# Performance work log

Measured on AMD Instinct MI355X. Metric: run time of the kernel, lower is better.

## Reference

```python
import jax, jax.numpy as jnp
import numpy as np

WIN = 12     # SAMv3 window_size
HEADS = 8    # num_heads

def _window(t, win=WIN):
    B, H, W, C = t.shape
    t = t.reshape(B, H // win, win, W // win, win, C).transpose(0, 1, 3, 2, 4, 5)
    return t.reshape(B, (H // win) * (W // win), win * win, C)

def _unwindow(t, H, W, win=WIN):
    B, nW, S, C = t.shape
    t = t.reshape(B, H // win, W // win, win, win, C).transpose(0, 1, 3, 2, 4, 5)
    return t.reshape(B, H, W, C)

def _sam(fq, fkv, bias, wq, wk, wv, wo, bo):
    # Windowed, masked cross-frame multi-head attention (SAMv3).
    # fq, fkv: (B, C, H, W); bias: (B, nW, 1, 1, S) additive mask bias.
    B, C, H, W = fq.shape
    hd = C // HEADS
    scale = hd ** -0.5
    q = _window(jnp.einsum('bchw,cd->bhwd', fq, wq))   # (B,nW,S,C)
    k = _window(jnp.einsum('bchw,cd->bhwd', fkv, wk))
    v = _window(jnp.einsum('bchw,cd->bhwd', fkv, wv))
    nW, S = q.shape[1], q.shape[2]
    q = q.reshape(B, nW, S, HEADS, hd)
    k = k.reshape(B, nW, S, HEADS, hd)
    v = v.reshape(B, nW, S, HEADS, hd)
    attn = jnp.einsum('bnqhd,bnkhd->bnhqk', q, k) * scale + bias
    attn = jax.nn.softmax(attn, axis=-1)
    out = jnp.einsum('bnhqk,bnkhd->bnqhd', attn, v).reshape(B, nW, S, C)
    out = out @ wo + bo
    return _unwindow(out, H, W).transpose(0, 3, 1, 2)  # (B, C, H, W)

def setup_inputs() -> dict:
    key = jax.random.key(0)
    B, C, T, H, W = 2, 384, 2, 192, 192
    ks = jax.random.split(key, 16)
    d = {}
    d['x'] = jax.random.normal(ks[0], (B, C, T, H, W), jnp.float32)
    d['mask'] = jax.random.randint(ks[1], (B, T, 1, H, W), 0, 2, jnp.int32)
    names = ['sam1_wq', 'sam1_wk', 'sam1_wv', 'sam1_wo',
             'sam2_wq', 'sam2_wk', 'sam2_wv', 'sam2_wo',
             'proj1_w', 'proj2_w']
    for i, n in enumerate(names):
        d[n] = jax.random.normal(ks[2 + i], (C, C), jnp.float32) * 0.02
    d['sam1_bo'] = jnp.zeros((C,), jnp.float32)
    d['sam2_bo'] = jnp.zeros((C,), jnp.float32)
    d['proj1_b'] = jnp.zeros((C,), jnp.float32)
    d['proj2_b'] = jnp.zeros((C,), jnp.float32)
    return d

def reference(x, mask, sam1_wq, sam1_wk, sam1_wv, sam1_wo, sam1_bo,
              sam2_wq, sam2_wk, sam2_wv, sam2_wo, sam2_bo,
              proj1_w, proj1_b, proj2_w, proj2_b):
    # x: (B, C, T=2, H, W); mask: (B, T, 1, H, W)
    f1 = x[:, :, 0]
    f2 = x[:, :, 1]
    m = mask[:, 1, 0][..., None]                      # (B, H, W, 1), frame-2 mask
    mw = _window(m)[..., 0]                           # (B, nW, S)
    bias = jnp.where(mw == 0, -1e9, 0.0).astype(x.dtype)[:, :, None, None, :]
    o1 = _sam(f1, f2, bias, sam1_wq, sam1_wk, sam1_wv, sam1_wo, sam1_bo)
    x1 = jnp.einsum('bchw,dc->bdhw', o1, proj1_w) + proj1_b[None, :, None, None]
    o2 = _sam(f2, f1, bias, sam2_wq, sam2_wk, sam2_wv, sam2_wo, sam2_bo)
    x2 = jnp.einsum('bchw,dc->bdhw', o2, proj2_w) + proj2_b[None, :, None, None]
    return jnp.concatenate([x1[:, :, None], x2[:, :, None]], axis=2)  # (B, C, 2, H, W)
```

## Files before the change

### kernel.cpp

```cpp
#include <hip/hip_runtime.h>
#include <stdint.h>

typedef __attribute__((ext_vector_type(8))) short bf16x8;
typedef __attribute__((ext_vector_type(4))) float f32x4;

#define HW    36864
#define CCH   384
#define NPIX  73728
#define W2    147456
#define NPAD  1280
#define WTF   491520

__device__ __forceinline__ unsigned short f2bf(float f) {
  unsigned u = __builtin_bit_cast(unsigned, f);
  u += 0x7FFFu + ((u >> 16) & 1u);
  return (unsigned short)(u >> 16);
}

typedef const unsigned int __attribute__((address_space(1)))* gas1_t;
typedef unsigned int __attribute__((address_space(3)))* las3_t;
__device__ __forceinline__ void gload16(const void* g, void* l) {
  __builtin_amdgcn_global_load_lds((gas1_t)g, (las3_t)l, 16, 0, 0);
}


__global__ void k_wt(const float* __restrict__ w0, const float* __restrict__ w1,
                     const float* __restrict__ w2, const float* __restrict__ w3,
                     const float* __restrict__ w4, const float* __restrict__ w5,
                     unsigned short* __restrict__ wt) {
  int idx = blockIdx.x * 256 + threadIdx.x;
  int w = blockIdx.y;
  const float* W;
  switch (w) { case 0: W = w0; break; case 1: W = w1; break;
               case 2: W = w2; break; case 3: W = w3; break;
               case 4: W = w4; break; default: W = w5; break; }
  const int fmap[6]    = {0, 1, 1, 1, 0, 0};
  const int basemap[6] = {0, 384, 768, 0, 384, 768};
  int c = idx / 384, d = idx % 384;
  wt[(size_t)fmap[w] * WTF + (size_t)(basemap[w] + d) * 384 + c] =
      f2bf(W[(size_t)c * 384 + d]);
}

__global__ void k_pad(unsigned short* __restrict__ wt) {
  int idx = blockIdx.x * 256 + threadIdx.x;
  int f = idx / 49152, rem = idx % 49152;
  wt[(size_t)f * WTF + 1152 * 384 + rem] = 0;
}

__global__ void k_wf(const float* __restrict__ wo1, const float* __restrict__ pj1,
                     const float* __restrict__ wo2, const float* __restrict__ pj2,
                     unsigned short* __restrict__ wfT) {
  int idx = blockIdx.x * 256 + threadIdx.x;
  int s = blockIdx.y;
  const float* wo = s ? wo2 : wo1;
  const float* pj = s ? pj2 : pj1;
  int d = idx / 384, e = idx % 384;
  float acc = 0.f;
  for (int c = 0; c < 384; ++c) acc += pj[d * 384 + c] * wo[e * 384 + c];
  wfT[(size_t)s * W2 + (size_t)d * 384 + e] = f2bf(acc);
}

__global__ void k_bf(const float* __restrict__ bo1, const float* __restrict__ pj1,
                     const float* __restrict__ pb1, const float* __restrict__ bo2,
                     const float* __restrict__ pj2, const float* __restrict__ pb2,
                     float* __restrict__ bfused) {
  int t = threadIdx.x;
  int s = t / 384, d = t % 384;
  const float* bo = s ? bo2 : bo1;
  const float* pj = s ? pj2 : pj1;
  const float* pb = s ? pb2 : pb1;
  float acc = pb[d];
  for (int c = 0; c < 384; ++c) acc += pj[d * 384 + c] * bo[c];
  bfused[t] = acc;
}

__global__ __launch_bounds__(256) void k_tx(const float* __restrict__ x,
                                            unsigned short* __restrict__ xbf) {
  __shared__ float tile[64][65];
  int p0 = blockIdx.x * 64;
  int c0 = blockIdx.y * 64;
  int bt = blockIdx.z;
  int b = bt >> 1, t = bt & 1;
  int tid = threadIdx.x;
  int cl = tid >> 2;
  int pq = (tid & 3) * 4;
  const float* src = x + (((size_t)b * CCH + (c0 + cl)) * 2 + t) * HW + p0;
#pragma unroll
  for (int i = 0; i < 4; ++i) {
    int p_l = pq + i * 16;
    float4 v = *reinterpret_cast<const float4*>(src + p_l);
    tile[cl][p_l + 0] = v.x; tile[cl][p_l + 1] = v.y;
    tile[cl][p_l + 2] = v.z; tile[cl][p_l + 3] = v.w;
  }
  __syncthreads();
  int pl = tid >> 2;
  int cq = (tid & 3) * 16;
  unsigned short* dst = xbf + ((size_t)(t * 2 + b) * HW + p0 + pl) * CCH + c0 + cq;
  bf16x8 o0, o1;
#pragma unroll
  for (int j = 0; j < 8; ++j) o0[j] = (short)f2bf(tile[cq + j][pl]);
#pragma unroll
  for (int j = 0; j < 8; ++j) o1[j] = (short)f2bf(tile[cq + 8 + j][pl]);
  *reinterpret_cast<bf16x8*>(dst) = o0;
  *reinterpret_cast<bf16x8*>(dst + 8) = o1;
}

__global__ __launch_bounds__(512) void gemm_qkv(
    const unsigned short* __restrict__ xbf,
    const unsigned short* __restrict__ wt,
    unsigned short* __restrict__ qb0,
    unsigned short* __restrict__ qb1,
    unsigned short* __restrict__ kvb0,
    unsigned short* __restrict__ kvb1,
    float oscale) {
  __shared__ __align__(16) unsigned short Lsh[2][32768];
  const int tid = threadIdx.x;
  const int lane = tid & 63;
  const int wid = tid >> 6;
  const int wr = wid >> 2, wc = wid & 3;
  const int r15 = lane & 15, g = lane >> 4;
  const int rsw = r15 & 7;

  const int gx = gridDim.x;
  const int nwg = gx * gridDim.y;
  const int bid = blockIdx.x + blockIdx.y * gx;
  const int chunk = nwg >> 3;
  const int l = (bid & 7) * chunk + (bid >> 3);
  const int bx = l % gx, by = l / gx;

  const int f = (by >= 288) ? 1 : 0;
  const int m0 = (by - f * 288) * 256;
  const int n0 = bx * 256;

  const unsigned short* A  = xbf + (size_t)f * NPIX * 384;
  const unsigned short* Bt = wt + (size_t)f * WTF;
  unsigned short* Cq  = f ? qb1 : qb0;
  unsigned short* Ckv = f ? kvb0 : kvb1;

  const int gsl = (tid & 7) ^ ((tid >> 3) & 7);
  const unsigned short* srcA = A + (size_t)(m0 + (tid >> 3)) * 384 + gsl * 8;
  const unsigned short* srcB = Bt + (size_t)(n0 + (tid >> 3)) * 384 + gsl * 8;

  f32x4 acc[8][4];
  f32x4 zero4 = {0.f, 0.f, 0.f, 0.f};
#pragma unroll
  for (int a = 0; a < 8; ++a)
#pragma unroll
    for (int b = 0; b < 4; ++b) acc[a][b] = zero4;

#define SA(buf, kt, q) gload16(srcA + (size_t)(q) * 64 * 384 + (kt) * 64, \
                               &Lsh[(buf)][tid * 8 + (q) * 4096])
#define SB(buf, kt, q) gload16(srcB + (size_t)(q) * 64 * 384 + (kt) * 64, \
                               &Lsh[(buf)][16384 + tid * 8 + (q) * 4096])

  bf16x8 af[4][2], bf[2][2];
#define LDA(buf, mh) do {                                                        \
    _Pragma("unroll")                                                            \
    for (int a = 0; a < 4; ++a) {                                                \
      int row = wr * 128 + (mh) * 64 + a * 16 + r15;                             \
      af[a][0] = *(const bf16x8*)&Lsh[(buf)][row * 64 + ((0 + g) ^ rsw) * 8];    \
      af[a][1] = *(const bf16x8*)&Lsh[(buf)][row * 64 + ((4 + g) ^ rsw) * 8];    \
    } } while (0)
#define LDB(buf, nh) do {                                                        \
    _Pragma("unroll")                                                            \
    for (int b = 0; b < 2; ++b) {                                                \
      int row = wc * 64 + (nh) * 32 + b * 16 + r15;                              \
      bf[b][0] = *(const bf16x8*)&Lsh[(buf)][16384 + row * 64 + ((0 + g) ^ rsw) * 8];\
      bf[b][1] = *(const bf16x8*)&Lsh[(buf)][16384 + row * 64 + ((4 + g) ^ rsw) * 8];\
    } } while (0)
#define MM(mh, nh) do {                                                          \
    __builtin_amdgcn_s_setprio(1);                                               \
    _Pragma("unroll")                                                            \
    for (int a = 0; a < 4; ++a)                                                  \
      _Pragma("unroll")                                                          \
      for (int b = 0; b < 2; ++b) {                                              \
        acc[(mh)*4+a][(nh)*2+b] = __builtin_amdgcn_mfma_f32_16x16x32_bf16(       \
            af[a][0], bf[b][0], acc[(mh)*4+a][(nh)*2+b], 0, 0, 0);               \
        acc[(mh)*4+a][(nh)*2+b] = __builtin_amdgcn_mfma_f32_16x16x32_bf16(       \
            af[a][1], bf[b][1], acc[(mh)*4+a][(nh)*2+b], 0, 0, 0);               \
      }                                                                          \
    __builtin_amdgcn_s_setprio(0);                                               \
  } while (0)

#define BAR() __builtin_amdgcn_s_barrier()
#define LGKM0() asm volatile("s_waitcnt lgkmcnt(0)" ::: "memory")

  SB(0, 0, 0); SB(0, 0, 1); SB(0, 0, 2); SB(0, 0, 3);
  SA(0, 0, 0); SA(0, 0, 2);
  SA(0, 0, 1); SA(0, 0, 3);
  asm volatile("s_waitcnt vmcnt(2)" ::: "memory");
  BAR();

#define TILE(kt, STG, W1STR, W3)                                              \
  do {                                                                        \
    const int c_ = (kt) & 1, s_ = c_ ^ 1;                                     \
    LDA(c_, 0); LDB(c_, 0);                                                   \
    if (STG) { SB(s_, (kt) + 1, 0); SB(s_, (kt) + 1, 1); }                    \
    BAR(); LGKM0(); MM(0, 0); BAR();                                          \
    LDB(c_, 1);                                                               \
    if (STG) { SB(s_, (kt) + 1, 2); SB(s_, (kt) + 1, 3); }                    \
    BAR(); LGKM0(); MM(0, 1);                                                 \
    asm volatile("s_waitcnt " W1STR ::: "memory");                            \
    BAR();                                                                    \
    LDA(c_, 1);                                                               \
    if (STG) { SA(s_, (kt) + 1, 0); SA(s_, (kt) + 1, 2); }                    \
    BAR(); LGKM0(); MM(1, 1); BAR();                                          \
    LDB(c_, 0);                                                               \
    if (STG) { SA(s_, (kt) + 1, 1); SA(s_, (kt) + 1, 3); }                    \
    BAR(); LGKM0(); MM(1, 0);                                                 \
    if (W3) { asm volatile("s_waitcnt vmcnt(2)" ::: "memory"); BAR(); }       \
  } while (0)

  TILE(0, 1, "vmcnt(4)", 1);
  TILE(1, 1, "vmcnt(4)", 1);
  TILE(2, 1, "vmcnt(4)", 1);
  TILE(3, 1, "vmcnt(4)", 1);
  TILE(4, 1, "vmcnt(4)", 1);
  TILE(5, 0, "vmcnt(0)", 0);
#undef TILE
#undef SA
#undef SB
#undef LDA
#undef LDB
#undef MM
#undef BAR
#undef LGKM0

#pragma unroll
  for (int a = 0; a < 8; ++a) {
    int m = m0 + wr * 128 + a * 16 + g * 4;
#pragma unroll
    for (int b = 0; b < 4; ++b) {
      int nbase = n0 + wc * 64 + b * 16;
      if (nbase < 384) {
        unsigned short* cp = Cq + (size_t)m * 384 + nbase + r15;
#pragma unroll
        for (int r = 0; r < 4; ++r) cp[(size_t)r * 384] = f2bf(acc[a][b][r] * oscale);
      } else if (nbase < 1152) {
        unsigned short* cp = Ckv + (size_t)m * 768 + (nbase - 384) + r15;
#pragma unroll
        for (int r = 0; r < 4; ++r) cp[(size_t)r * 768] = f2bf(acc[a][b][r]);
      }
    }
  }
}

__global__ __launch_bounds__(256) void gemm_out(
    const unsigned short* __restrict__ wfT,
    const unsigned short* __restrict__ ob0,
    const unsigned short* __restrict__ ob1,
    float* __restrict__ Cf,
    const float* __restrict__ bfu) {
  __shared__ __align__(16) unsigned short Lsh[3][8192];
  const int tid = threadIdx.x;
  const int lane = tid & 63;
  const int wid = tid >> 6, wr = wid >> 1, wc = wid & 1;

  const int gx = gridDim.x, gy = gridDim.y;
  const int nwg = gx * gy * gridDim.z;
  const int bid = blockIdx.x + (blockIdx.y + blockIdx.z * gy) * gx;
  const int chunk = nwg >> 3;
  const int l = (bid & 7) * chunk + (bid >> 3);
  const int bx = l % gx;
  const int by = (l / gx) % gy;
  const int s  = l / (gx * gy);

  const unsigned short* A  = wfT + (size_t)s * W2;
  const unsigned short* Bt = s ? ob1 : ob0;
  const float* bias = bfu + s * 384;

  const int m0 = bx * 128;
  const int n0 = by * 128;
  const int r15 = lane & 15, g = lane >> 4;

  const int u1 = tid + 256;
  const unsigned short* srcA0 = A + (size_t)(m0 + (tid >> 2)) * 384 + (((tid & 3) ^ ((tid >> 3) & 3)) << 3);
  const unsigned short* srcA1 = A + (size_t)(m0 + (u1 >> 2)) * 384 + (((u1 & 3) ^ ((u1 >> 3) & 3)) << 3);
  const unsigned short* srcB0 = Bt + (size_t)(n0 + (tid >> 2)) * 384 + (((tid & 3) ^ ((tid >> 3) & 3)) << 3);
  const unsigned short* srcB1 = Bt + (size_t)(n0 + (u1 >> 2)) * 384 + (((u1 & 3) ^ ((u1 >> 3) & 3)) << 3);
  const int wbase = (tid & ~63) * 8;

  f32x4 acc[4][4];
  f32x4 zero4 = {0.f, 0.f, 0.f, 0.f};
#pragma unroll
  for (int a = 0; a < 4; ++a)
#pragma unroll
    for (int b = 0; b < 4; ++b) acc[a][b] = zero4;

  const int swzr = (g ^ ((r15 >> 1) & 3)) << 3;

#define STAGE(buf, kt) do {                                  \
    int ke = (kt) * 32;                                      \
    gload16(srcA0 + ke, &Lsh[(buf)][wbase]);                 \
    gload16(srcA1 + ke, &Lsh[(buf)][2048 + wbase]);          \
    gload16(srcB0 + ke, &Lsh[(buf)][4096 + wbase]);          \
    gload16(srcB1 + ke, &Lsh[(buf)][6144 + wbase]);          \
  } while (0)

#define COMPUTE(buf) do {                                                       \
    bf16x8 af[4], bfv[4];                                                       \
    _Pragma("unroll")                                                           \
    for (int a = 0; a < 4; ++a)                                                 \
      af[a] = *(const bf16x8*)&Lsh[(buf)][(wr * 64 + a * 16 + r15) * 32 + swzr];\
    _Pragma("unroll")                                                           \
    for (int b = 0; b < 4; ++b)                                                 \
      bfv[b] = *(const bf16x8*)&Lsh[(buf)][4096 + (wc * 64 + b * 16 + r15) * 32 + swzr];\
    _Pragma("unroll")                                                           \
    for (int a = 0; a < 4; ++a)                                                 \
      _Pragma("unroll")                                                         \
      for (int b = 0; b < 4; ++b)                                               \
        acc[a][b] = __builtin_amdgcn_mfma_f32_16x16x32_bf16(af[a], bfv[b], acc[a][b], 0, 0, 0);\
  } while (0)

  STAGE(0, 0);
  STAGE(1, 1);
#pragma unroll
  for (int kt = 0; kt < 11; ++kt) {
    asm volatile("s_waitcnt vmcnt(4)" ::: "memory");
    __builtin_amdgcn_s_barrier();
    asm volatile("" ::: "memory");
    if (kt < 10) STAGE((kt + 2) % 3, kt + 2);
    COMPUTE(kt % 3);
  }
  __syncthreads();
  COMPUTE(11 % 3);
#undef STAGE
#undef COMPUTE

  int bb = n0 / HW;
#pragma unroll
  for (int a = 0; a < 4; ++a) {
    int d = m0 + wr * 64 + a * 16 + g * 4;
#pragma unroll
    for (int b = 0; b < 4; ++b) {
      int n = n0 + wc * 64 + b * 16 + r15;
      int p = n - bb * HW;
#pragma unroll
      for (int r = 0; r < 4; ++r) {
        float v = acc[a][b][r] + bias[d + r];
        Cf[(((size_t)bb * CCH + (d + r)) * 2 + s) * HW + p] = v;
      }
    }
  }
}

__global__ __launch_bounds__(512, 2) void attn_kernel(
    const unsigned short* __restrict__ qb0,
    const unsigned short* __restrict__ qb1,
    const unsigned short* __restrict__ kvb0,
    const unsigned short* __restrict__ kvb1,
    const int* __restrict__ mask,
    unsigned short* __restrict__ ob0,
    unsigned short* __restrict__ ob1) {
  __shared__ __align__(16) unsigned short P[8][16][168];
  __shared__ int ptab[144];
  const int n = blockIdx.x, b = blockIdx.y, s = blockIdx.z;
  const unsigned short* q  = s ? qb1 : qb0;
  const unsigned short* kv = s ? kvb1 : kvb0;
  unsigned short* obuf = s ? ob1 : ob0;
  const int tid = threadIdx.x;
  const int h = tid >> 6, lane = tid & 63;
  const int c15 = lane & 15, g = lane >> 4;
  const int wy = n >> 4, wx = n & 15;
  const size_t rowbase = (size_t)b * HW;
  const int* mrow = mask + (size_t)(b * 2 + 1) * HW;

  if (tid < 144)
    ptab[tid] = (wy * 12 + tid / 12) * 192 + wx * 12 + tid % 12;

  for (int idx = lane; idx < 16 * 24; idx += 64)
    P[h][idx / 24][144 + (idx % 24)] = 0;
  __syncthreads();

  float biasv[9];
#pragma unroll
  for (int nt = 0; nt < 9; ++nt)
    biasv[nt] = (mrow[ptab[nt * 16 + c15]] == 0) ? -1e9f : 0.0f;

  bf16x8 zfrag = {0, 0, 0, 0, 0, 0, 0, 0};
  f32x4 zero4 = {0.f, 0.f, 0.f, 0.f};

  bf16x8 kf0[9], kf1[9];
#pragma unroll
  for (int nt = 0; nt < 9; ++nt) {
    const unsigned short* kp = kv + (rowbase + ptab[nt * 16 + c15]) * 768 + h * 48;
    kf0[nt] = *(const bf16x8*)(kp + g * 8);
    kf1[nt] = zfrag;
    if (g < 2) kf1[nt] = *(const bf16x8*)(kp + 32 + g * 8);
  }

  const unsigned short* vb = kv + rowbase * 768 + 384 + h * 48;
  bf16x8 vf[5][3];
#pragma unroll
  for (int ks = 0; ks < 5; ++ks) {
#pragma unroll
    for (int dt = 0; dt < 3; ++dt) {
      bf16x8 v = {0, 0, 0, 0, 0, 0, 0, 0};
#pragma unroll
      for (int j = 0; j < 8; ++j) {
        int sk = ks * 32 + g * 8 + j;
        if (sk < 144)
          v[j] = (short)vb[(size_t)ptab[sk] * 768 + dt * 16 + c15];
      }
      vf[ks][dt] = v;
    }
  }

  bf16x8 qf0, qf1;
  {
    const unsigned short* qp = q + (rowbase + ptab[c15]) * 384 + h * 48;
    qf0 = *(const bf16x8*)(qp + g * 8);
    qf1 = zfrag;
    if (g < 2) qf1 = *(const bf16x8*)(qp + 32 + g * 8);
  }

  for (int mt = 0; mt < 9; ++mt) {
    bf16x8 qn0 = zfrag, qn1 = zfrag;
    if (mt < 8) {
      const unsigned short* qp = q + (rowbase + ptab[(mt + 1) * 16 + c15]) * 384 + h * 48;
      qn0 = *(const bf16x8*)(qp + g * 8);
      if (g < 2) qn1 = *(const bf16x8*)(qp + 32 + g * 8);
    }

    float l4[4] = {0.f, 0.f, 0.f, 0.f};
    f32x4 oacc[3];
#pragma unroll
    for (int dt = 0; dt < 3; ++dt) oacc[dt] = zero4;

#pragma unroll
    for (int nt = 0; nt < 9; ++nt) {
      f32x4 sv = __builtin_amdgcn_mfma_f32_16x16x32_bf16(qf1, kf1[nt], zero4, 0, 0, 0);
      sv = __builtin_amdgcn_mfma_f32_16x16x32_bf16(qf0, kf0[nt], sv, 0, 0, 0);
#pragma unroll
      for (int r = 0; r < 4; ++r) {
        float pv = __expf(sv[r] + biasv[nt]);
        l4[r] += pv;
        P[h][g * 4 + r][nt * 16 + c15] = f2bf(pv);
      }
      if (nt & 1) {
        int ks = nt >> 1;
        bf16x8 pf = *(const bf16x8*)&P[h][c15][ks * 32 + g * 8];
#pragma unroll
        for (int dt = 0; dt < 3; ++dt)
          oacc[dt] = __builtin_amdgcn_mfma_f32_16x16x32_bf16(pf, vf[ks][dt], oacc[dt], 0, 0, 0);
      }
    }
    {
      bf16x8 pf = *(const bf16x8*)&P[h][c15][4 * 32 + g * 8];
#pragma unroll
      for (int dt = 0; dt < 3; ++dt)
        oacc[dt] = __builtin_amdgcn_mfma_f32_16x16x32_bf16(pf, vf[4][dt], oacc[dt], 0, 0, 0);
    }

#pragma unroll
    for (int st = 1; st < 16; st <<= 1)
#pragma unroll
      for (int r = 0; r < 4; ++r) l4[r] += __shfl_xor(l4[r], st, 64);

    float inv[4];
#pragma unroll
    for (int r = 0; r < 4; ++r) inv[r] = 1.0f / l4[r];
#pragma unroll
    for (int dt = 0; dt < 3; ++dt) {
#pragma unroll
      for (int r = 0; r < 4; ++r) {
        int so = mt * 16 + g * 4 + r;
        obuf[(rowbase + ptab[so]) * 384 + h * 48 + dt * 16 + c15] =
            f2bf(oacc[dt][r] * inv[r]);
      }
    }

    qf0 = qn0; qf1 = qn1;
  }
}

extern "C" void kernel_launch(void* const* d_in, const int* in_sizes, int n_in,
                              void* d_out, int out_size, void* d_ws, size_t ws_size,
                              hipStream_t stream) {
  const float* x    = (const float*)d_in[0];
  const int*   mask = (const int*)d_in[1];
  const float* wq1 = (const float*)d_in[2];
  const float* wk1 = (const float*)d_in[3];
  const float* wv1 = (const float*)d_in[4];
  const float* wo1 = (const float*)d_in[5];
  const float* wq2 = (const float*)d_in[6];
  const float* wk2 = (const float*)d_in[7];
  const float* wv2 = (const float*)d_in[8];
  const float* wo2 = (const float*)d_in[9];
  const float* pj1 = (const float*)d_in[10];
  const float* pj2 = (const float*)d_in[11];
  const float* bo1 = (const float*)d_in[12];
  const float* bo2 = (const float*)d_in[13];
  const float* pb1 = (const float*)d_in[14];
  const float* pb2 = (const float*)d_in[15];
  float* out = (float*)d_out;

  const float SCALE = 0.14433756729740643f;

  char* ws = (char*)d_ws;
  size_t off = 0;
  unsigned short* wt   = (unsigned short*)(ws + off); off += (size_t)2 * WTF * 2;
  unsigned short* wfT  = (unsigned short*)(ws + off); off += (size_t)2 * W2 * 2;
  float*          bfu  = (float*)(ws + off);          off += (size_t)2 * 384 * 4;
  unsigned short* xbf  = (unsigned short*)(ws + off); off += (size_t)4 * HW * CCH * 2;
  size_t qsz = (size_t)NPIX * 384 * 2, kvsz = (size_t)NPIX * 768 * 2;
  unsigned short* qb0  = (unsigned short*)(ws + off); off += qsz;
  unsigned short* qb1  = (unsigned short*)(ws + off); off += qsz;
  unsigned short* kvb0 = (unsigned short*)(ws + off); off += kvsz;
  unsigned short* kvb1 = (unsigned short*)(ws + off); off += kvsz;
  unsigned short* ob0  = (unsigned short*)(ws + off); off += qsz;
  unsigned short* ob1  = (unsigned short*)(ws + off); off += qsz;
  if (ws_size < off) return;

  k_wt<<<dim3(576, 6), 256, 0, stream>>>(wq1, wk1, wv1, wq2, wk2, wv2, wt);
  k_pad<<<384, 256, 0, stream>>>(wt);
  k_wf<<<dim3(576, 2), 256, 0, stream>>>(wo1, pj1, wo2, pj2, wfT);
  k_bf<<<1, 768, 0, stream>>>(bo1, pj1, pb1, bo2, pj2, pb2, bfu);
  k_tx<<<dim3(576, 6, 4), 256, 0, stream>>>(x, xbf);

  gemm_qkv<<<dim3(5, 576), 512, 0, stream>>>(xbf, wt, qb0, qb1, kvb0, kvb1, SCALE);
  attn_kernel<<<dim3(256, 2, 2), 512, 0, stream>>>(qb0, qb1, kvb0, kvb1, mask, ob0, ob1);
  gemm_out<<<dim3(3, 576, 2), 256, 0, stream>>>(wfT, ob0, ob1, out, bfu);
}
```

Measured before the change: 661.5 us.

## Make QKV GEMM persistent over 12 M-tiles with cross-tile prefetch

Result: slower. 951.6 us (+43.9%).

```diff
diff --git a/kernel.cpp b/kernel.cpp
--- a/kernel.cpp
+++ b/kernel.cpp
@@ -128,8 +128,9 @@
   const int l = (bid & 7) * chunk + (bid >> 3);
   const int bx = l % gx, by = l / gx;
 
-  const int f = (by >= 288) ? 1 : 0;
-  const int m0 = (by - f * 288) * 256;
+  const int f = (by >= 24) ? 1 : 0;
+  const int mg = by - f * 24;
+  const int mbase = mg * 3072;
   const int n0 = bx * 256;
 
   const unsigned short* A  = xbf + (size_t)f * NPIX * 384;
@@ -138,7 +139,7 @@
   unsigned short* Ckv = f ? kvb0 : kvb1;
 
   const int gsl = (tid & 7) ^ ((tid >> 3) & 7);
-  const unsigned short* srcA = A + (size_t)(m0 + (tid >> 3)) * 384 + gsl * 8;
+  const unsigned short* srcA = A + (size_t)(mbase + (tid >> 3)) * 384 + gsl * 8;
   const unsigned short* srcB = Bt + (size_t)(n0 + (tid >> 3)) * 384 + gsl * 8;
 
   f32x4 acc[8][4];
@@ -148,12 +149,12 @@
 #pragma unroll
     for (int b = 0; b < 4; ++b) acc[a][b] = zero4;
 
-#define SA(buf, kt, q) gload16(srcA + (size_t)(q) * 64 * 384 + (kt) * 64, \
-                               &Lsh[(buf)][tid * 8 + (q) * 4096])
-#define SB(buf, kt, q) gload16(srcB + (size_t)(q) * 64 * 384 + (kt) * 64, \
-                               &Lsh[(buf)][16384 + tid * 8 + (q) * 4096])
-
-  bf16x8 af[4][2], bf[2][2];
+#define SAq(buf, src, ko, q) gload16((src) + (size_t)(q) * 64 * 384 + (ko), \
+                                     &Lsh[(buf)][tid * 8 + (q) * 4096])
+#define SBq(buf, ko, q) gload16(srcB + (size_t)(q) * 64 * 384 + (ko), \
+                                &Lsh[(buf)][16384 + tid * 8 + (q) * 4096])
+
+  bf16x8 af[4][2], bf_lo[2][2], bf_hi[2][2];
 #define LDA(buf, mh) do {                                                        \
     _Pragma("unroll")                                                            \
     for (int a = 0; a < 4; ++a) {                                                \
@@ -161,23 +162,23 @@
       af[a][0] = *(const bf16x8*)&Lsh[(buf)][row * 64 + ((0 + g) ^ rsw) * 8];    \
       af[a][1] = *(const bf16x8*)&Lsh[(buf)][row * 64 + ((4 + g) ^ rsw) * 8];    \
     } } while (0)
-#define LDB(buf, nh) do {                                                        \
+#define LDB(buf, nh, DST) do {                                                   \
     _Pragma("unroll")                                                            \
     for (int b = 0; b < 2; ++b) {                                                \
       int row = wc * 64 + (nh) * 32 + b * 16 + r15;                              \
-      bf[b][0] = *(const bf16x8*)&Lsh[(buf)][16384 + row * 64 + ((0 + g) ^ rsw) * 8];\
-      bf[b][1] = *(const bf16x8*)&Lsh[(buf)][16384 + row * 64 + ((4 + g) ^ rsw) * 8];\
+      DST[b][0] = *(const bf16x8*)&Lsh[(buf)][16384 + row * 64 + ((0 + g) ^ rsw) * 8];\
+      DST[b][1] = *(const bf16x8*)&Lsh[(buf)][16384 + row * 64 + ((4 + g) ^ rsw) * 8];\
     } } while (0)
-#define MM(mh, nh) do {                                                          \
+#define MM(mh, nh, BF) do {                                                      \
     __builtin_amdgcn_s_setprio(1);                                               \
     _Pragma("unroll")                                                            \
     for (int a = 0; a < 4; ++a)                                                  \
       _Pragma("unroll")                                                          \
       for (int b = 0; b < 2; ++b) {                                              \
         acc[(mh)*4+a][(nh)*2+b] = __builtin_amdgcn_mfma_f32_16x16x32_bf16(       \
-            af[a][0], bf[b][0], acc[(mh)*4+a][(nh)*2+b], 0, 0, 0);               \
+            af[a][0], BF[b][0], acc[(mh)*4+a][(nh)*2+b], 0, 0, 0);               \
         acc[(mh)*4+a][(nh)*2+b] = __builtin_amdgcn_mfma_f32_16x16x32_bf16(       \
-            af[a][1], bf[b][1], acc[(mh)*4+a][(nh)*2+b], 0, 0, 0);               \
+            af[a][1], BF[b][1], acc[(mh)*4+a][(nh)*2+b], 0, 0, 0);               \
       }                                                                          \
     __builtin_amdgcn_s_setprio(0);                                               \
   } while (0)
@@ -185,64 +186,87 @@
 #define BAR() __builtin_amdgcn_s_barrier()
 #define LGKM0() asm volatile("s_waitcnt lgkmcnt(0)" ::: "memory")
 
-  SB(0, 0, 0); SB(0, 0, 1); SB(0, 0, 2); SB(0, 0, 3);
-  SA(0, 0, 0); SA(0, 0, 2);
-  SA(0, 0, 1); SA(0, 0, 3);
+#define TILE_STEADY(kt, ASRC, KO2) do {                                       \
+    constexpr int c_ = (kt) & 1, s_ = c_ ^ 1;                                 \
+    LDA(c_, 0); LDB(c_, 0, bf_lo);                                            \
+    SBq(s_, (KO2), 0); SBq(s_, (KO2), 1);                                     \
+    BAR(); LGKM0(); MM(0, 0, bf_lo); BAR();                                   \
+    LDB(c_, 1, bf_hi);                                                        \
+    SBq(s_, (KO2), 2); SBq(s_, (KO2), 3);                                     \
+    BAR(); LGKM0(); MM(0, 1, bf_hi);                                          \
+    asm volatile("s_waitcnt vmcnt(4)" ::: "memory");                          \
+    BAR();                                                                    \
+    LDA(c_, 1);                                                               \
+    SAq(s_, (ASRC), (KO2), 0); SAq(s_, (ASRC), (KO2), 2);                     \
+    BAR(); LGKM0(); MM(1, 1, bf_hi); BAR();                                   \
+    SAq(s_, (ASRC), (KO2), 1); SAq(s_, (ASRC), (KO2), 3);                     \
+    BAR(); MM(1, 0, bf_lo);                                                   \
+    asm volatile("s_waitcnt vmcnt(2)" ::: "memory");                          \
+    BAR();                                                                    \
+  } while (0)
+
+  SBq(0, 0, 0); SBq(0, 0, 1); SBq(0, 0, 2); SBq(0, 0, 3);
+  SAq(0, srcA, 0, 0); SAq(0, srcA, 0, 2);
+  SAq(0, srcA, 0, 1); SAq(0, srcA, 0, 3);
   asm volatile("s_waitcnt vmcnt(2)" ::: "memory");
   BAR();
 
-#define TILE(kt, STG, W1STR, W3)                                              \
-  do {                                                                        \
-    const int c_ = (kt) & 1, s_ = c_ ^ 1;                                     \
-    LDA(c_, 0); LDB(c_, 0);                                                   \
-    if (STG) { SB(s_, (kt) + 1, 0); SB(s_, (kt) + 1, 1); }                    \
-    BAR(); LGKM0(); MM(0, 0); BAR();                                          \
-    LDB(c_, 1);                                                               \
-    if (STG) { SB(s_, (kt) + 1, 2); SB(s_, (kt) + 1, 3); }                    \
-    BAR(); LGKM0(); MM(0, 1);                                                 \
-    asm volatile("s_waitcnt " W1STR ::: "memory");                            \
-    BAR();                                                                    \
-    LDA(c_, 1);                                                               \
-    if (STG) { SA(s_, (kt) + 1, 0); SA(s_, (kt) + 1, 2); }                    \
-    BAR(); LGKM0(); MM(1, 1); BAR();                                          \
-    LDB(c_, 0);                                                               \
-    if (STG) { SA(s_, (kt) + 1, 1); SA(s_, (kt) + 1, 3); }                    \
-    BAR(); LGKM0(); MM(1, 0);                                                 \
-    if (W3) { asm volatile("s_waitcnt vmcnt(2)" ::: "memory"); BAR(); }       \
-  } while (0)
-
-  TILE(0, 1, "vmcnt(4)", 1);
-  TILE(1, 1, "vmcnt(4)", 1);
-  TILE(2, 1, "vmcnt(4)", 1);
-  TILE(3, 1, "vmcnt(4)", 1);
-  TILE(4, 1, "vmcnt(4)", 1);
-  TILE(5, 0, "vmcnt(0)", 0);
-#undef TILE
-#undef SA
-#undef SB
+#pragma unroll 1
+  for (int mt = 0; mt < 12; ++mt) {
+    const unsigned short* srcAn = srcA + 98304;
+
+    TILE_STEADY(0, srcA, 1 * 64);
+    TILE_STEADY(1, srcA, 2 * 64);
+    TILE_STEADY(2, srcA, 3 * 64);
+    TILE_STEADY(3, srcA, 4 * 64);
+    TILE_STEADY(4, srcA, 5 * 64);
+    if (mt < 11) {
+      TILE_STEADY(5, srcAn, 0);
+    } else {
+      LDA(1, 0); LDB(1, 0, bf_lo);
+      BAR(); LGKM0(); MM(0, 0, bf_lo); BAR();
+      LDB(1, 1, bf_hi);
+      BAR(); LGKM0(); MM(0, 1, bf_hi);
+      asm volatile("s_waitcnt vmcnt(0)" ::: "memory");
+      BAR();
+      LDA(1, 1);
+      BAR(); LGKM0(); MM(1, 1, bf_hi); MM(1, 0, bf_lo);
+    }
+
+    {
+      const int m0 = mbase + mt * 256;
+#pragma unroll
+      for (int a = 0; a < 8; ++a) {
+        int m = m0 + wr * 128 + a * 16 + g * 4;
+#pragma unroll
+        for (int b = 0; b < 4; ++b) {
+          int nbase = n0 + wc * 64 + b * 16;
+          if (nbase < 384) {
+            unsigned short* cp = Cq + (size_t)m * 384 + nbase + r15;
+#pragma unroll
+            for (int r = 0; r < 4; ++r) cp[(size_t)r * 384] = f2bf(acc[a][b][r] * oscale);
+          } else if (nbase < 1152) {
+            unsigned short* cp = Ckv + (size_t)m * 768 + (nbase - 384) + r15;
+#pragma unroll
+            for (int r = 0; r < 4; ++r) cp[(size_t)r * 768] = f2bf(acc[a][b][r]);
+          }
+        }
+      }
+#pragma unroll
+      for (int a = 0; a < 8; ++a)
+#pragma unroll
+        for (int b = 0; b < 4; ++b) acc[a][b] = zero4;
+    }
+    srcA = srcAn;
+  }
+#undef TILE_STEADY
+#undef SAq
+#undef SBq
 #undef LDA
 #undef LDB
 #undef MM
 #undef BAR
 #undef LGKM0
-
-#pragma unroll
-  for (int a = 0; a < 8; ++a) {
-    int m = m0 + wr * 128 + a * 16 + g * 4;
-#pragma unroll
-    for (int b = 0; b < 4; ++b) {
-      int nbase = n0 + wc * 64 + b * 16;
-      if (nbase < 384) {
-        unsigned short* cp = Cq + (size_t)m * 384 + nbase + r15;
-#pragma unroll
-        for (int r = 0; r < 4; ++r) cp[(size_t)r * 384] = f2bf(acc[a][b][r] * oscale);
-      } else if (nbase < 1152) {
-        unsigned short* cp = Ckv + (size_t)m * 768 + (nbase - 384) + r15;
-#pragma unroll
-        for (int r = 0; r < 4; ++r) cp[(size_t)r * 768] = f2bf(acc[a][b][r]);
-      }
-    }
-  }
 }
 
 __global__ __launch_bounds__(256) void gemm_out(
@@ -518,7 +542,7 @@
   k_bf<<<1, 768, 0, stream>>>(bo1, pj1, pb1, bo2, pj2, pb2, bfu);
   k_tx<<<dim3(576, 6, 4), 256, 0, stream>>>(x, xbf);
 
-  gemm_qkv<<<dim3(5, 576), 512, 0, stream>>>(xbf, wt, qb0, qb1, kvb0, kvb1, SCALE);
+  gemm_qkv<<<dim3(5, 48), 512, 0, stream>>>(xbf, wt, qb0, qb1, kvb0, kvb1, SCALE);
   attn_kernel<<<dim3(256, 2, 2), 512, 0, stream>>>(qb0, qb1, kvb0, kvb1, mask, ob0, ob1);
   gemm_out<<<dim3(3, 576, 2), 256, 0, stream>>>(wfT, ob0, ob1, out, bfu);
 }
```
